# Kernel tuning notes

Measured on AMD Instinct MI355X. Metric: run time of the kernel, lower is better.

The kernel has to match this reference:

```python
import jax, jax.numpy as jnp
import numpy as np

N_NODES = 100000


def gcn_conv(x, W, b, src, dst, num_nodes):
    # PyG GCNConv: add self-loops, symmetric deg^-1/2 normalization,
    # linear transform, scatter-add aggregation at dst, then bias.
    loop = jnp.arange(num_nodes, dtype=src.dtype)
    row = jnp.concatenate([src, loop])  # message sources
    col = jnp.concatenate([dst, loop])  # message destinations
    deg = jax.ops.segment_sum(jnp.ones_like(col, dtype=x.dtype), col,
                              num_segments=num_nodes)
    dinv = jnp.where(deg > 0, jax.lax.rsqrt(deg), 0.0)
    norm = dinv[row] * dinv[col]  # [E+N]
    h = x @ W  # [N, out]
    msg = h[row] * norm[:, None]  # gather + scale, [E+N, out]
    out = jax.ops.segment_sum(msg, col, num_segments=num_nodes)  # scatter-add
    return out + b


def setup_inputs() -> dict:
    key = jax.random.key(0)
    k1, k2, k3, k4, k5, k6 = jax.random.split(key, 6)
    dim_in, dim_h = 256, 128
    E = 1600000
    x = jax.random.normal(k1, (N_NODES, dim_in), dtype=jnp.float32)
    edge_index = jax.random.randint(k2, (2, E), 0, N_NODES, dtype=jnp.int64)
    # Glorot-style init for GCNConv weights
    W1 = jax.random.normal(k3, (dim_in, dim_h), dtype=jnp.float32) * (1.0 / np.sqrt(dim_in))
    b1 = jnp.zeros((dim_h,), dtype=jnp.float32)
    W2 = jax.random.normal(k4, (dim_h, 1), dtype=jnp.float32) * (1.0 / np.sqrt(dim_h))
    b2 = jnp.zeros((1,), dtype=jnp.float32)
    return {"x": x, "edge_index": edge_index, "W1": W1, "b1": b1, "W2": W2, "b2": b2}


def reference(x, edge_index, W1, b1, W2, b2):
    src, dst = edge_index[0], edge_index[1]
    h = gcn_conv(x, W1, b1, src, dst, N_NODES)
    h = jax.nn.relu(h)
    h = gcn_conv(h, W2, b2, src, dst, N_NODES)
    return jax.nn.sigmoid(h)  # [N, 1]
```

## Files before the change

### kernel.cpp

```cpp
#include <hip/hip_runtime.h>
#include <math.h>

#define NN 100000
#define DIN 256
#define DH 128
#define GEMM_NB 1563
#define BSHIFT 9
#define BNODES 512
#define NB_BUCKET 196
#define BCAP 12288
#define PA_EDGES 4096
#define PREP_NB 64

#define QSCL (5.0f / 127.0f)
#define QINV (127.0f / 5.0f)

using short8  = __attribute__((ext_vector_type(8))) short;
using float4v = __attribute__((ext_vector_type(4))) float;

static __device__ __forceinline__ unsigned short f2bf(float f) {
    unsigned u = __float_as_uint(f);
    unsigned r = u + 0x7fffu + ((u >> 16) & 1u);
    return (unsigned short)(r >> 16);
}

__global__ __launch_bounds__(512) void k_prep_partA(const float* __restrict__ W1,
                                                    unsigned short* __restrict__ W1p,
                                                    const int* __restrict__ src,
                                                    const int* __restrict__ dst, int E,
                                                    int* __restrict__ bucketFill,
                                                    unsigned* __restrict__ bucketArr) {
    __shared__ int aCnt[NB_BUCKET];
    __shared__ int aBase[NB_BUCKET];
    const int tid = threadIdx.x;

    if (blockIdx.x < PREP_NB) {
        int t = blockIdx.x * 512 + tid;
        int lane = t & 63;
        int ks   = (t >> 6) & 7;
        int nt   = (t >> 9) & 1;
        int wv   = (t >> 10) & 3;
        int n = wv * 32 + nt * 16 + (lane & 15);
        int kbase = ks * 32 + (lane >> 4) * 8;
        short8 v;
#pragma unroll
        for (int j = 0; j < 8; ++j) v[j] = (short)f2bf(W1[(kbase + j) * DH + n]);
        *(short8*)&W1p[(long long)t * 8] = v;
        return;
    }

    const int ba = blockIdx.x - PREP_NB;
    for (int i = tid; i < NB_BUCKET; i += 512) aCnt[i] = 0;
    __syncthreads();
    const int e0   = ba * PA_EDGES;
    const int eend = min(e0 + PA_EDGES, E);
    for (int e = e0 + tid; e < eend; e += 512) {
        int d = __builtin_nontemporal_load(&dst[e]);
        atomicAdd(&aCnt[d >> BSHIFT], 1);
    }
    __syncthreads();
    for (int i = tid; i < NB_BUCKET; i += 512) {
        int c = aCnt[i];
        aBase[i] = c ? atomicAdd(&bucketFill[i], c) : 0;
        aCnt[i] = 0;
    }
    __syncthreads();
    for (int e = e0 + tid; e < eend; e += 512) {
        int d = __builtin_nontemporal_load(&dst[e]);
        int s = __builtin_nontemporal_load(&src[e]);
        int b = d >> BSHIFT;
        int r = atomicAdd(&aCnt[b], 1);
        bucketArr[(long long)b * BCAP + aBase[b] + r] =
            ((unsigned)(d & (BNODES - 1)) << 17) | (unsigned)s;
    }
}

__global__ __launch_bounds__(512) void k_gemm_partB(const float* __restrict__ x,
                                                    const unsigned short* __restrict__ W1p,
                                                    unsigned* __restrict__ hs8,
                                                    const int* __restrict__ bucketFill,
                                                    const unsigned* __restrict__ bucketArr,
                                                    int* __restrict__ cnt,
                                                    int* __restrict__ excl,
                                                    float* __restrict__ dinv,
                                                    int* __restrict__ eidx) {
    __shared__ unsigned short aL[64 * 32 * 8];
    __shared__ int h[BNODES];
    __shared__ int hex[BNODES];
    __shared__ int st[256];
    const int tid = threadIdx.x;

    if (blockIdx.x < NB_BUCKET) {
        const int b     = blockIdx.x;
        const int nbase = b << BSHIFT;
        const int len   = bucketFill[b];
        const long long abase = (long long)b * BCAP;

        if (tid < 256) st[tid] = (tid < b) ? bucketFill[tid] : 0;
        __syncthreads();
        for (int off = 128; off > 0; off >>= 1) {
            if (tid < off) st[tid] += st[tid + off];
            __syncthreads();
        }
        const int gbase = st[0];
        __syncthreads();

        for (int i = tid; i < BNODES; i += 512) h[i] = 0;
        __syncthreads();
        for (int k = tid; k < len; k += 512)
            atomicAdd(&h[bucketArr[abase + k] >> 17], 1);
        __syncthreads();

        int a0 = 0, a1 = 0;
        if (tid < 256) {
            a0 = h[2 * tid]; a1 = h[2 * tid + 1];
            st[tid] = a0 + a1;
        }
        __syncthreads();
        for (int off = 1; off < 256; off <<= 1) {
            int val = (tid < 256 && tid >= off) ? st[tid - off] : 0;
            __syncthreads();
            if (tid < 256) st[tid] += val;
            __syncthreads();
        }
        if (tid < 256) {
            int prev = (tid > 0) ? st[tid - 1] : 0;
            hex[2 * tid]     = prev;
            hex[2 * tid + 1] = prev + a0;
        }
        __syncthreads();

        for (int i = tid; i < BNODES; i += 512) {
            int n = nbase + i;
            if (n < NN) {
                int c = h[i];
                cnt[n]  = c;
                excl[n] = gbase + hex[i];
                dinv[n] = rsqrtf(1.0f + (float)c);
            }
        }
        for (int i = tid; i < BNODES; i += 512) h[i] = 0;
        __syncthreads();

        for (int k = tid; k < len; k += 512) {
            unsigned p = bucketArr[abase + k];
            int li = p >> 17;
            int r = atomicAdd(&h[li], 1);
            eidx[gbase + hex[li] + r] = (int)(p & 0x1FFFFu);
        }
        return;
    }

    const int bid  = blockIdx.x - NB_BUCKET;
    const int w8   = tid >> 6;
    const int lane = tid & 63;
    const int quad = lane >> 4;
    const int m16  = lane & 15;
    const int row0 = bid * 64;

    short8 bfr[8];
#pragma unroll
    for (int ks = 0; ks < 8; ++ks)
        bfr[ks] = ((const short8*)W1p)[(w8 * 8 + ks) * 64 + lane];

#pragma unroll
    for (int it = 0; it < 4; ++it) {
        int id  = it * 512 + tid;
        int row = id >> 5;
        int kb  = id & 31;
        int gr  = row0 + row;
        float4v f0, f1;
        if (gr < NN) {
            const float4v* xp = (const float4v*)&x[(long long)gr * DIN + kb * 8];
            f0 = __builtin_nontemporal_load(xp);
            f1 = __builtin_nontemporal_load(xp + 1);
        } else {
            f0 = (float4v)(0.0f);
            f1 = (float4v)(0.0f);
        }
        short8 v;
        v[0] = (short)f2bf(f0[0]); v[1] = (short)f2bf(f0[1]);
        v[2] = (short)f2bf(f0[2]); v[3] = (short)f2bf(f0[3]);
        v[4] = (short)f2bf(f1[0]); v[5] = (short)f2bf(f1[1]);
        v[6] = (short)f2bf(f1[2]); v[7] = (short)f2bf(f1[3]);
        int chunk = row * 32 + (kb ^ (row & 31));
        *(short8*)&aL[chunk * 8] = v;
    }
    __syncthreads();

    float4v acc[4];
#pragma unroll
    for (int mt = 0; mt < 4; ++mt) acc[mt] = (float4v)(0.0f);

#pragma unroll
    for (int mt = 0; mt < 4; ++mt) {
        int row = mt * 16 + m16;
#pragma unroll
        for (int ks = 0; ks < 8; ++ks) {
            int kb = ks * 4 + quad;
            int chunk = row * 32 + (kb ^ (row & 31));
            short8 a = *(const short8*)&aL[chunk * 8];
            acc[mt] = __builtin_amdgcn_mfma_f32_16x16x32_bf16(a, bfr[ks], acc[mt], 0, 0, 0);
        }
    }

#pragma unroll
    for (int mt = 0; mt < 4; ++mt) {
#pragma unroll
        for (int r = 0; r < 4; ++r) {
            int row = row0 + mt * 16 + quad * 4 + r;
            float hq = fminf(fmaxf(acc[mt][r] * QINV, -127.0f), 127.0f);
            unsigned b = (unsigned)((int)rintf(hq)) & 0xffu;
            unsigned v01 = b | (((unsigned)__shfl_down((int)b, 1)) << 8);
            unsigned v   = v01 | (((unsigned)__shfl_down((int)v01, 2)) << 16);
            if ((m16 & 3) == 0 && row < NN)
                hs8[row * 32 + w8 * 4 + (m16 >> 2)] = v;
        }
    }
}

__global__ __launch_bounds__(256) void k_agg1l2(const int* __restrict__ eidx,
                                                const int* __restrict__ excl,
                                                const int* __restrict__ cnt,
                                                const unsigned* __restrict__ hs8,
                                                const float* __restrict__ dinv,
                                                const float* __restrict__ b1,
                                                const float* __restrict__ W2,
                                                float* __restrict__ zs) {
    int w = (blockIdx.x * 256 + threadIdx.x) >> 6;
    if (w >= NN) return;
    const int lane = threadIdx.x & 63;
    const int hh   = lane >> 5;
    const int l5   = lane & 31;
    int offs = excl[w];
    int c    = cnt[w];

    float dw = dinv[w];

    unsigned su = hs8[(long long)w * 32 + l5];
    float ss = hh ? 0.0f : dw * QSCL;
    float a0 = ss * (float)(int)(char)(su);
    float a1 = ss * (float)(int)(char)(su >> 8);
    float a2 = ss * (float)(int)(char)(su >> 16);
    float a3 = ss * (float)(int)(char)(su >> 24);

    int j = 0;
    for (; j + 7 < c; j += 8) {
        int s[4]; float es[4]; unsigned uu[4];
#pragma unroll
        for (int q = 0; q < 4; ++q) s[q] = eidx[offs + j + 2 * q + hh];
#pragma unroll
        for (int q = 0; q < 4; ++q) es[q] = dinv[s[q]] * QSCL;
#pragma unroll
        for (int q = 0; q < 4; ++q) uu[q] = hs8[(long long)s[q] * 32 + l5];
#pragma unroll
        for (int q = 0; q < 4; ++q) {
            a0 = fmaf(es[q], (float)(int)(char)(uu[q]), a0);
            a1 = fmaf(es[q], (float)(int)(char)(uu[q] >> 8), a1);
            a2 = fmaf(es[q], (float)(int)(char)(uu[q] >> 16), a2);
            a3 = fmaf(es[q], (float)(int)(char)(uu[q] >> 24), a3);
        }
    }
    for (; j + 1 < c; j += 2) {
        int s0 = eidx[offs + j + hh];
        float e0 = dinv[s0] * QSCL;
        unsigned u0 = hs8[(long long)s0 * 32 + l5];
        a0 = fmaf(e0, (float)(int)(char)(u0), a0);
        a1 = fmaf(e0, (float)(int)(char)(u0 >> 8), a1);
        a2 = fmaf(e0, (float)(int)(char)(u0 >> 16), a2);
        a3 = fmaf(e0, (float)(int)(char)(u0 >> 24), a3);
    }
    if (j < c) {
        int s0 = eidx[offs + j];
        float e0 = hh ? 0.0f : dinv[s0] * QSCL;
        unsigned u0 = hs8[(long long)s0 * 32 + l5];
        a0 = fmaf(e0, (float)(int)(char)(u0), a0);
        a1 = fmaf(e0, (float)(int)(char)(u0 >> 8), a1);
        a2 = fmaf(e0, (float)(int)(char)(u0 >> 16), a2);
        a3 = fmaf(e0, (float)(int)(char)(u0 >> 24), a3);
    }

    a0 += __shfl_xor(a0, 32);
    a1 += __shfl_xor(a1, 32);
    a2 += __shfl_xor(a2, 32);
    a3 += __shfl_xor(a3, 32);

    float4 bb = ((const float4*)b1)[l5];
    float4 ww = ((const float4*)W2)[l5];
    float r0 = fmaxf(fmaf(dw, a0, bb.x), 0.0f);
    float r1 = fmaxf(fmaf(dw, a1, bb.y), 0.0f);
    float r2 = fmaxf(fmaf(dw, a2, bb.z), 0.0f);
    float r3 = fmaxf(fmaf(dw, a3, bb.w), 0.0f);
    float v = r0 * ww.x + r1 * ww.y + r2 * ww.z + r3 * ww.w;
#pragma unroll
    for (int off = 16; off > 0; off >>= 1) v += __shfl_down(v, off);
    if (lane == 0) zs[w] = v * dw;
}

__global__ void k_agg2_final(const int* __restrict__ eidx,
                             const int* __restrict__ excl,
                             const int* __restrict__ cnt,
                             const float* __restrict__ zs,
                             const float* __restrict__ dinv,
                             const float* __restrict__ b2,
                             float* __restrict__ out) {
    int i = blockIdx.x * 256 + threadIdx.x;
    if (i >= NN) return;
    int offs = excl[i];
    int c = cnt[i];
    float v = zs[i];
    int j = 0;
    for (; j + 3 < c; j += 4) {
        int s0 = __builtin_nontemporal_load(&eidx[offs + j + 0]);
        int s1 = __builtin_nontemporal_load(&eidx[offs + j + 1]);
        int s2 = __builtin_nontemporal_load(&eidx[offs + j + 2]);
        int s3 = __builtin_nontemporal_load(&eidx[offs + j + 3]);
        v += zs[s0] + zs[s1] + zs[s2] + zs[s3];
    }
    for (; j < c; ++j) v += zs[eidx[offs + j]];
    float z = fmaf(dinv[i], v, b2[0]);
    out[i] = 1.0f / (1.0f + __expf(-z));
}

extern "C" void kernel_launch(void* const* d_in, const int* in_sizes, int n_in,
                              void* d_out, int out_size, void* d_ws, size_t ws_size,
                              hipStream_t stream) {
    const float* x  = (const float*)d_in[0];
    const int*   ei = (const int*)d_in[1];
    const float* W1 = (const float*)d_in[2];
    const float* b1 = (const float*)d_in[3];
    const float* W2 = (const float*)d_in[4];
    const float* b2 = (const float*)d_in[5];
    float* out = (float*)d_out;

    const int E = in_sizes[1] / 2;
    const int* src = ei;
    const int* dst = ei + E;

    int* wsi = (int*)d_ws;
    float* dinv       = (float*)wsi;
    int*   cnt        = wsi + NN;
    int*   excl       = cnt + NN;
    float* zs         = (float*)(excl + NN);
    int*   bucketFill = (int*)(zs + NN);
    unsigned short* W1p = (unsigned short*)(bucketFill + 256);
    int*   eidx       = (int*)(W1p + 32768);
    unsigned* bucketArr = (unsigned*)(eidx + E);
    unsigned* hs8     = bucketArr + (long long)NB_BUCKET * BCAP;

    const int nb_nodes = (NN + 255) / 256;
    const int pa_nb = (E + PA_EDGES - 1) / PA_EDGES;

    hipMemsetAsync(bucketFill, 0, NB_BUCKET * sizeof(int), stream);

    k_prep_partA<<<PREP_NB + pa_nb, 512, 0, stream>>>(W1, W1p, src, dst, E,
                                                      bucketFill, bucketArr);
    k_gemm_partB<<<NB_BUCKET + GEMM_NB, 512, 0, stream>>>(x, W1p, hs8, bucketFill, bucketArr,
                                                          cnt, excl, dinv, eidx);

    k_agg1l2<<<(NN * 64 + 255) / 256, 256, 0, stream>>>(eidx, excl, cnt,
                                                        hs8, dinv, b1, W2, zs);

    k_agg2_final<<<nb_nodes, 256, 0, stream>>>(eidx, excl, cnt, zs, dinv, b2, out);
}
```

Before: 281.6 us.

## Stage bucketed edges in LDS and widen agg1 gathers to 8-byte rows

The edge bucketing kernel now keeps 8192 edges per block in registers, computes local bucket offsets with a prefix scan, stages the packed entries in shared memory sorted by bucket, and then writes each bucket's run contiguously to global memory. Before, each edge was scattered individually to global memory. The layer-1 aggregation now has each 16-lane quarter of a wave gather one neighbor's whole 128-byte int8 row as uint2 loads, handling 8 edges per iteration with clamped, masked tails. This replaces the 32-lane halves with 4-byte loads. The changes trade extra registers, a 32 KB shared staging buffer and more shuffle reductions for fewer, wider and more coalesced memory transactions.

```diff
diff --git a/kernel.cpp b/kernel.cpp
--- a/kernel.cpp
+++ b/kernel.cpp
@@ -9,7 +9,7 @@
 #define BNODES 512
 #define NB_BUCKET 196
 #define BCAP 12288
-#define PA_EDGES 4096
+#define PA_EDGES 8192
 #define PREP_NB 64
 
 #define QSCL (5.0f / 127.0f)
@@ -23,6 +23,10 @@
     unsigned r = u + 0x7fffu + ((u >> 16) & 1u);
     return (unsigned short)(r >> 16);
 }
+static __device__ __forceinline__ float i8f0(unsigned u) { return (float)(int)(char)(u); }
+static __device__ __forceinline__ float i8f1(unsigned u) { return (float)(int)(char)(u >> 8); }
+static __device__ __forceinline__ float i8f2(unsigned u) { return (float)(int)(char)(u >> 16); }
+static __device__ __forceinline__ float i8f3(unsigned u) { return (float)(int)(char)(u >> 24); }
 
 __global__ __launch_bounds__(512) void k_prep_partA(const float* __restrict__ W1,
                                                     unsigned short* __restrict__ W1p,
@@ -31,7 +35,11 @@
                                                     int* __restrict__ bucketFill,
                                                     unsigned* __restrict__ bucketArr) {
     __shared__ int aCnt[NB_BUCKET];
+    __shared__ int aCur[NB_BUCKET];
     __shared__ int aBase[NB_BUCKET];
+    __shared__ int lex[NB_BUCKET];
+    __shared__ int tmp[256];
+    __shared__ unsigned stg[PA_EDGES];
     const int tid = threadIdx.x;
 
     if (blockIdx.x < PREP_NB) {
@@ -49,29 +57,58 @@
         return;
     }
 
-    const int ba = blockIdx.x - PREP_NB;
-    for (int i = tid; i < NB_BUCKET; i += 512) aCnt[i] = 0;
-    __syncthreads();
+    const int ba   = blockIdx.x - PREP_NB;
     const int e0   = ba * PA_EDGES;
     const int eend = min(e0 + PA_EDGES, E);
-    for (int e = e0 + tid; e < eend; e += 512) {
-        int d = __builtin_nontemporal_load(&dst[e]);
-        atomicAdd(&aCnt[d >> BSHIFT], 1);
-    }
-    __syncthreads();
-    for (int i = tid; i < NB_BUCKET; i += 512) {
-        int c = aCnt[i];
-        aBase[i] = c ? atomicAdd(&bucketFill[i], c) : 0;
-        aCnt[i] = 0;
-    }
-    __syncthreads();
-    for (int e = e0 + tid; e < eend; e += 512) {
-        int d = __builtin_nontemporal_load(&dst[e]);
-        int s = __builtin_nontemporal_load(&src[e]);
-        int b = d >> BSHIFT;
-        int r = atomicAdd(&aCnt[b], 1);
-        bucketArr[(long long)b * BCAP + aBase[b] + r] =
-            ((unsigned)(d & (BNODES - 1)) << 17) | (unsigned)s;
+
+    int dR[16], sR[16];
+#pragma unroll
+    for (int i = 0; i < 16; ++i) {
+        int e = e0 + i * 512 + tid;
+        if (e < eend) {
+            dR[i] = __builtin_nontemporal_load(&dst[e]);
+            sR[i] = __builtin_nontemporal_load(&src[e]);
+        } else dR[i] = -1;
+    }
+
+    for (int i = tid; i < NB_BUCKET; i += 512) { aCnt[i] = 0; aCur[i] = 0; }
+    __syncthreads();
+#pragma unroll
+    for (int i = 0; i < 16; ++i)
+        if (dR[i] >= 0) atomicAdd(&aCnt[dR[i] >> BSHIFT], 1);
+    __syncthreads();
+
+    int cb = (tid < NB_BUCKET) ? aCnt[tid] : 0;
+    if (tid < 256) tmp[tid] = cb;
+    __syncthreads();
+    for (int off = 1; off < 256; off <<= 1) {
+        int v = (tid < 256 && tid >= off) ? tmp[tid - off] : 0;
+        __syncthreads();
+        if (tid < 256) tmp[tid] += v;
+        __syncthreads();
+    }
+    if (tid < NB_BUCKET) {
+        lex[tid]   = tmp[tid] - cb;
+        aBase[tid] = cb ? atomicAdd(&bucketFill[tid], cb) : 0;
+    }
+    __syncthreads();
+
+#pragma unroll
+    for (int i = 0; i < 16; ++i)
+        if (dR[i] >= 0) {
+            int b = dR[i] >> BSHIFT;
+            int r = atomicAdd(&aCur[b], 1);
+            stg[lex[b] + r] = ((unsigned)(dR[i] & (BNODES - 1)) << 17) | (unsigned)sR[i];
+        }
+    __syncthreads();
+
+    const int wv = tid >> 6, ln = tid & 63;
+    for (int b = wv; b < NB_BUCKET; b += 8) {
+        int c  = aCur[b];
+        int l0 = lex[b];
+        long long g0 = (long long)b * BCAP + aBase[b];
+        for (int k = ln; k < c; k += 64)
+            bucketArr[g0 + k] = stg[l0 + k];
     }
 }
 
@@ -230,70 +267,64 @@
     int w = (blockIdx.x * 256 + threadIdx.x) >> 6;
     if (w >= NN) return;
     const int lane = threadIdx.x & 63;
-    const int hh   = lane >> 5;
-    const int l5   = lane & 31;
+    const int qq   = lane >> 4;
+    const int l4   = lane & 15;
     int offs = excl[w];
     int c    = cnt[w];
 
     float dw = dinv[w];
-
-    unsigned su = hs8[(long long)w * 32 + l5];
-    float ss = hh ? 0.0f : dw * QSCL;
-    float a0 = ss * (float)(int)(char)(su);
-    float a1 = ss * (float)(int)(char)(su >> 8);
-    float a2 = ss * (float)(int)(char)(su >> 16);
-    float a3 = ss * (float)(int)(char)(su >> 24);
-
-    int j = 0;
-    for (; j + 7 < c; j += 8) {
-        int s[4]; float es[4]; unsigned uu[4];
-#pragma unroll
-        for (int q = 0; q < 4; ++q) s[q] = eidx[offs + j + 2 * q + hh];
-#pragma unroll
-        for (int q = 0; q < 4; ++q) es[q] = dinv[s[q]] * QSCL;
-#pragma unroll
-        for (int q = 0; q < 4; ++q) uu[q] = hs8[(long long)s[q] * 32 + l5];
-#pragma unroll
-        for (int q = 0; q < 4; ++q) {
-            a0 = fmaf(es[q], (float)(int)(char)(uu[q]), a0);
-            a1 = fmaf(es[q], (float)(int)(char)(uu[q] >> 8), a1);
-            a2 = fmaf(es[q], (float)(int)(char)(uu[q] >> 16), a2);
-            a3 = fmaf(es[q], (float)(int)(char)(uu[q] >> 24), a3);
-        }
-    }
-    for (; j + 1 < c; j += 2) {
-        int s0 = eidx[offs + j + hh];
-        float e0 = dinv[s0] * QSCL;
-        unsigned u0 = hs8[(long long)s0 * 32 + l5];
-        a0 = fmaf(e0, (float)(int)(char)(u0), a0);
-        a1 = fmaf(e0, (float)(int)(char)(u0 >> 8), a1);
-        a2 = fmaf(e0, (float)(int)(char)(u0 >> 16), a2);
-        a3 = fmaf(e0, (float)(int)(char)(u0 >> 24), a3);
-    }
-    if (j < c) {
-        int s0 = eidx[offs + j];
-        float e0 = hh ? 0.0f : dinv[s0] * QSCL;
-        unsigned u0 = hs8[(long long)s0 * 32 + l5];
-        a0 = fmaf(e0, (float)(int)(char)(u0), a0);
-        a1 = fmaf(e0, (float)(int)(char)(u0 >> 8), a1);
-        a2 = fmaf(e0, (float)(int)(char)(u0 >> 16), a2);
-        a3 = fmaf(e0, (float)(int)(char)(u0 >> 24), a3);
-    }
-
-    a0 += __shfl_xor(a0, 32);
-    a1 += __shfl_xor(a1, 32);
-    a2 += __shfl_xor(a2, 32);
-    a3 += __shfl_xor(a3, 32);
-
-    float4 bb = ((const float4*)b1)[l5];
-    float4 ww = ((const float4*)W2)[l5];
-    float r0 = fmaxf(fmaf(dw, a0, bb.x), 0.0f);
-    float r1 = fmaxf(fmaf(dw, a1, bb.y), 0.0f);
-    float r2 = fmaxf(fmaf(dw, a2, bb.z), 0.0f);
-    float r3 = fmaxf(fmaf(dw, a3, bb.w), 0.0f);
-    float v = r0 * ww.x + r1 * ww.y + r2 * ww.z + r3 * ww.w;
-#pragma unroll
-    for (int off = 16; off > 0; off >>= 1) v += __shfl_down(v, off);
+    const uint2* hr = (const uint2*)hs8;
+
+    uint2 su = hr[w * 16 + l4];
+    float ss = (qq == 0) ? dw * QSCL : 0.0f;
+    float a0 = ss * i8f0(su.x), a1 = ss * i8f1(su.x), a2 = ss * i8f2(su.x), a3 = ss * i8f3(su.x);
+    float a4 = ss * i8f0(su.y), a5 = ss * i8f1(su.y), a6 = ss * i8f2(su.y), a7 = ss * i8f3(su.y);
+
+    const int cm1 = c - 1;
+    for (int j = 0; j < c; j += 8) {
+        int eq0 = j + qq;
+        int eq1 = j + 4 + qq;
+        int s0 = eidx[offs + min(eq0, cm1)];
+        int s1 = eidx[offs + min(eq1, cm1)];
+        float e0 = (eq0 < c) ? dinv[s0] * QSCL : 0.0f;
+        float e1 = (eq1 < c) ? dinv[s1] * QSCL : 0.0f;
+        uint2 u0 = hr[s0 * 16 + l4];
+        uint2 u1 = hr[s1 * 16 + l4];
+        a0 = fmaf(e0, i8f0(u0.x), a0); a1 = fmaf(e0, i8f1(u0.x), a1);
+        a2 = fmaf(e0, i8f2(u0.x), a2); a3 = fmaf(e0, i8f3(u0.x), a3);
+        a4 = fmaf(e0, i8f0(u0.y), a4); a5 = fmaf(e0, i8f1(u0.y), a5);
+        a6 = fmaf(e0, i8f2(u0.y), a6); a7 = fmaf(e0, i8f3(u0.y), a7);
+        a0 = fmaf(e1, i8f0(u1.x), a0); a1 = fmaf(e1, i8f1(u1.x), a1);
+        a2 = fmaf(e1, i8f2(u1.x), a2); a3 = fmaf(e1, i8f3(u1.x), a3);
+        a4 = fmaf(e1, i8f0(u1.y), a4); a5 = fmaf(e1, i8f1(u1.y), a5);
+        a6 = fmaf(e1, i8f2(u1.y), a6); a7 = fmaf(e1, i8f3(u1.y), a7);
+    }
+
+    a0 += __shfl_xor(a0, 16); a1 += __shfl_xor(a1, 16);
+    a2 += __shfl_xor(a2, 16); a3 += __shfl_xor(a3, 16);
+    a4 += __shfl_xor(a4, 16); a5 += __shfl_xor(a5, 16);
+    a6 += __shfl_xor(a6, 16); a7 += __shfl_xor(a7, 16);
+    a0 += __shfl_xor(a0, 32); a1 += __shfl_xor(a1, 32);
+    a2 += __shfl_xor(a2, 32); a3 += __shfl_xor(a3, 32);
+    a4 += __shfl_xor(a4, 32); a5 += __shfl_xor(a5, 32);
+    a6 += __shfl_xor(a6, 32); a7 += __shfl_xor(a7, 32);
+
+    float4 bb0 = ((const float4*)b1)[2 * l4];
+    float4 bb1 = ((const float4*)b1)[2 * l4 + 1];
+    float4 ww0 = ((const float4*)W2)[2 * l4];
+    float4 ww1 = ((const float4*)W2)[2 * l4 + 1];
+    float v = fmaxf(fmaf(dw, a0, bb0.x), 0.0f) * ww0.x
+            + fmaxf(fmaf(dw, a1, bb0.y), 0.0f) * ww0.y
+            + fmaxf(fmaf(dw, a2, bb0.z), 0.0f) * ww0.z
+            + fmaxf(fmaf(dw, a3, bb0.w), 0.0f) * ww0.w
+            + fmaxf(fmaf(dw, a4, bb1.x), 0.0f) * ww1.x
+            + fmaxf(fmaf(dw, a5, bb1.y), 0.0f) * ww1.y
+            + fmaxf(fmaf(dw, a6, bb1.z), 0.0f) * ww1.z
+            + fmaxf(fmaf(dw, a7, bb1.w), 0.0f) * ww1.w;
+    v += __shfl_xor(v, 1);
+    v += __shfl_xor(v, 2);
+    v += __shfl_xor(v, 4);
+    v += __shfl_xor(v, 8);
     if (lane == 0) zs[w] = v * dw;
 }
 
```

Result: no change. 279.5 us (-0.7%).
